# Optimization experiments

Hardware: AMD Instinct MI355X
Metric: run time of the kernel (lower is better)

Reference implementation:

```python
import jax, jax.numpy as jnp
import numpy as np
import math

N_HEAD = 16
EPS = 1e-5
GELU_C = math.sqrt(2.0 / math.pi)

def _layernorm(v, w):
    # LN with weight only (bias=None), matching the module's quirky constructor
    mu = jnp.mean(v, axis=-1, keepdims=True)
    var = jnp.mean(jnp.square(v - mu), axis=-1, keepdims=True)
    return (v - mu) * jax.lax.rsqrt(var + EPS) * w

def _new_gelu(x):
    return 0.5 * x * (1.0 + jnp.tanh(GELU_C * (x + 0.044715 * x ** 3)))

def setup_inputs() -> dict:
    key = jax.random.key(0)
    k1, k2, k3, k4 = jax.random.split(key, 4)
    B, T, C = 2, 2048, 2048
    x = jax.random.normal(k1, (B, T, C), dtype=jnp.float32)
    w_qkv = jax.random.normal(k2, (C, 3 * C), dtype=jnp.float32) * 0.02
    w1 = jax.random.normal(k3, (C, 4 * C), dtype=jnp.float32) * 0.02
    w2 = jax.random.normal(k4, (4 * C, C), dtype=jnp.float32) * 0.02
    ln_w = jnp.ones((C,), dtype=jnp.float32)
    return {"x": x, "w_qkv": w_qkv, "w1": w1, "w2": w2, "ln_w": ln_w}

def reference(x, w_qkv, w1, w2, ln_w):
    B, T, C = x.shape
    H = N_HEAD
    D = C // H
    # --- attention branch (pre-LN, shared ln weight) ---
    h = _layernorm(x, ln_w)
    qkv = h @ w_qkv  # [B,T,3C]
    q, k, v = jnp.split(qkv, 3, axis=-1)
    q = q.reshape(B, T, H, D)
    k = k.reshape(B, T, H, D)
    v = v.reshape(B, T, H, D)
    scale = 1.0 / math.sqrt(D)
    att = jnp.einsum('bthd,bshd->bhts', q, k) * scale  # [B,H,T,T]
    causal = jnp.tril(jnp.ones((T, T), dtype=bool))
    att = jnp.where(causal, att, -jnp.inf)
    att = jax.nn.softmax(att, axis=-1)
    attn_out = jnp.einsum('bhts,bshd->bthd', att, v).reshape(B, T, C)
    x = x + attn_out  # note: no output projection in this module
    # --- MLP branch (same ln weight reused) ---
    h2 = _layernorm(x, ln_w)
    mlp = _new_gelu(h2 @ w1) @ w2
    return x + mlp
```

## Files before the change

### kernel.cpp

```cpp
#include <hip/hip_runtime.h>
#include <hip/hip_bf16.h>
#include <math.h>

typedef __bf16 BF16;
typedef __attribute__((ext_vector_type(8))) __bf16 bf16x8;
typedef __attribute__((ext_vector_type(4))) float f32x4;

__device__ __forceinline__ void gld_lds16(const void* g, void* l) {
    __builtin_amdgcn_global_load_lds(
        (__attribute__((address_space(1))) void*)(const void*)g,
        (__attribute__((address_space(3))) void*)l, 16, 0, 0);
}

template <int N> __device__ __forceinline__ void vmwait() {
    asm volatile("s_waitcnt vmcnt(%0)" :: "i"(N));
}

__device__ __forceinline__ void SBAR() {
    __builtin_amdgcn_sched_barrier(0);
    __builtin_amdgcn_s_barrier();
    __builtin_amdgcn_sched_barrier(0);
}

__global__ __launch_bounds__(256) void lnorm(const float* __restrict__ x,
                                             const float* __restrict__ w,
                                             BF16* __restrict__ out) {
    const int row = blockIdx.x, tid = threadIdx.x;
    const float* xr = x + (size_t)row * 2048;
    float4 a = *(const float4*)(xr + tid * 8);
    float4 b = *(const float4*)(xr + tid * 8 + 4);
    float s1 = a.x + a.y + a.z + a.w + b.x + b.y + b.z + b.w;
    float s2 = a.x*a.x + a.y*a.y + a.z*a.z + a.w*a.w +
               b.x*b.x + b.y*b.y + b.z*b.z + b.w*b.w;
    #pragma unroll
    for (int off = 32; off; off >>= 1) {
        s1 += __shfl_xor(s1, off);
        s2 += __shfl_xor(s2, off);
    }
    __shared__ float red[8];
    const int l = tid & 63, wv = tid >> 6;
    if (l == 0) { red[wv] = s1; red[4 + wv] = s2; }
    __syncthreads();
    s1 = red[0] + red[1] + red[2] + red[3];
    s2 = red[4] + red[5] + red[6] + red[7];
    const float mean = s1 * (1.0f / 2048.0f);
    const float var  = s2 * (1.0f / 2048.0f) - mean * mean;
    const float rstd = rsqrtf(var + 1e-5f);
    float4 wa = *(const float4*)(w + tid * 8);
    float4 wb = *(const float4*)(w + tid * 8 + 4);
    bf16x8 o;
    o[0] = (BF16)((a.x - mean) * rstd * wa.x);
    o[1] = (BF16)((a.y - mean) * rstd * wa.y);
    o[2] = (BF16)((a.z - mean) * rstd * wa.z);
    o[3] = (BF16)((a.w - mean) * rstd * wa.w);
    o[4] = (BF16)((b.x - mean) * rstd * wb.x);
    o[5] = (BF16)((b.y - mean) * rstd * wb.y);
    o[6] = (BF16)((b.z - mean) * rstd * wb.z);
    o[7] = (BF16)((b.w - mean) * rstd * wb.w);
    *(bf16x8*)(out + (size_t)row * 2048 + tid * 8) = o;
}

__global__ __launch_bounds__(256) void wtrans(const float* __restrict__ W,
                                              BF16* __restrict__ Wt,
                                              int K, int N) {
    __shared__ BF16 tile[32][33];
    const int n0 = blockIdx.x * 32, k0 = blockIdx.y * 32;
    const int tx = threadIdx.x, ty = threadIdx.y;
    #pragma unroll
    for (int i = 0; i < 4; i++)
        tile[ty + 8 * i][tx] = (BF16)W[(size_t)(k0 + ty + 8 * i) * N + n0 + tx];
    __syncthreads();
    #pragma unroll
    for (int i = 0; i < 4; i++)
        Wt[(size_t)(n0 + ty + 8 * i) * K + k0 + tx] = tile[tx][ty + 8 * i];
}

__global__ __launch_bounds__(256) void vtrans(const BF16* __restrict__ qkv,
                                              BF16* __restrict__ vT) {
    __shared__ BF16 tile[32][33];
    const int t0 = blockIdx.x * 32, d0 = blockIdx.y * 32, bh = blockIdx.z;
    const int b = bh >> 4, h = bh & 15;
    const int tx = threadIdx.x, ty = threadIdx.y;
    const BF16* src = qkv + (size_t)b * 2048 * 6144 + 4096 + h * 128;
    #pragma unroll
    for (int i = 0; i < 4; i++)
        tile[ty + 8 * i][tx] = src[(size_t)(t0 + ty + 8 * i) * 6144 + d0 + tx];
    __syncthreads();
    BF16* dst = vT + (size_t)bh * 128 * 2048;
    #pragma unroll
    for (int i = 0; i < 4; i++)
        dst[(size_t)(d0 + ty + 8 * i) * 2048 + t0 + tx] = tile[tx][ty + 8 * i];
}


#define STA(SI, KK, TS) do { \
    _Pragma("unroll") \
    for (int j_ = 0; j_ < 2; ++j_) { \
        const int r_ = j_ * 128 + (tid >> 2); \
        const int sl_ = (tid & 3) ^ ((r_ >> 1) & 3); \
        gld_lds16(A + (size_t)(m0 + r_) * K + (TS) * 64 + (KK) * 32 + sl_ * 8, \
                  Ab + (SI) * 32768 + (KK) * 16384 + j_ * 8192 + w * 1024); \
    } \
} while (0)

#define STB(SI, KK, TS) do { \
    _Pragma("unroll") \
    for (int j_ = 0; j_ < LBU; ++j_) { \
        const int r_ = j_ * 128 + (tid >> 2); \
        const int sl_ = (tid & 3) ^ ((r_ >> 1) & 3); \
        gld_lds16(Bt + (size_t)(n0 + r_) * K + (TS) * 64 + (KK) * 32 + sl_ * 8, \
                  Bb + (SI) * BBUF + (KK) * (BN * 64) + j_ * 8192 + w * 1024); \
    } \
} while (0)

#define LDA(BI, MH, M_, KK) \
    (*(const bf16x8*)(Ab + (BI) * 32768 + (KK) * 16384 + \
        ((MH) * 128 + wm * 64 + (M_) * 16 + c) * 64 + ((g ^ fa) << 4)))

#define LDB(BI, N_, KK) \
    (*(const bf16x8*)(Bb + (BI) * BBUF + (KK) * (BN * 64) + \
        (wn * (BN / 4) + (N_) * 16 + c) * 64 + ((g ^ fa) << 4)))

#define MFMA_CL(MH) do { \
    __builtin_amdgcn_s_setprio(1); \
    _Pragma("unroll") \
    for (int m_ = 0; m_ < 4; ++m_) \
      _Pragma("unroll") \
      for (int n_ = 0; n_ < NR; ++n_) \
        acc[(MH) * 4 + m_][n_] = __builtin_amdgcn_mfma_f32_16x16x32_bf16( \
            af[m_], bfr[n_], acc[(MH) * 4 + m_][n_], 0, 0, 0); \
    __builtin_amdgcn_s_setprio(0); \
} while (0)

#define GBODY(BI, T, ST) do { \
    bf16x8 af[4], bfr[NR]; \
    _Pragma("unroll") for (int n_ = 0; n_ < NR; ++n_) bfr[n_] = LDB(BI, n_, 0); \
    _Pragma("unroll") for (int m_ = 0; m_ < 4; ++m_) af[m_] = LDA(BI, 0, m_, 0); \
    if (ST) STB((BI) ^ 1, 0, (T) + 1); \
    SBAR(); \
    MFMA_CL(0); \
    SBAR(); \
    _Pragma("unroll") for (int m_ = 0; m_ < 4; ++m_) af[m_] = LDA(BI, 1, m_, 0); \
    if (ST) STA((BI) ^ 1, 0, (T) + 1); \
    SBAR(); \
    MFMA_CL(1); \
    if (ST) vmwait<LBU + 2>(); else vmwait<0>(); \
    SBAR(); \
    _Pragma("unroll") for (int n_ = 0; n_ < NR; ++n_) bfr[n_] = LDB(BI, n_, 1); \
    _Pragma("unroll") for (int m_ = 0; m_ < 4; ++m_) af[m_] = LDA(BI, 0, m_, 1); \
    if (ST) STB((BI) ^ 1, 1, (T) + 1); \
    SBAR(); \
    MFMA_CL(0); \
    SBAR(); \
    _Pragma("unroll") for (int m_ = 0; m_ < 4; ++m_) af[m_] = LDA(BI, 1, m_, 1); \
    if (ST) STA((BI) ^ 1, 1, (T) + 1); \
    SBAR(); \
    MFMA_CL(1); \
    if (ST) vmwait<LBU + 2>(); \
    SBAR(); \
} while (0)

template <int MODE, int BN>
__global__ __launch_bounds__(512) void gemmT(const BF16* __restrict__ A,
                                             const BF16* __restrict__ Bt,
                                             void* __restrict__ out,
                                             const float* __restrict__ resid,
                                             int M, int N, int K) {
    constexpr int NR   = BN / 64;
    constexpr int LBU  = BN / 128;
    constexpr int BBUF = BN * 128;
    (void)M;

    extern __shared__ char smem[];
    char* const Ab = smem;
    char* const Bb = smem + 65536;

    const int tid = threadIdx.x, l = tid & 63, w = tid >> 6;
    const int wm = w >> 2, wn = w & 3;
    const int g = l >> 4, c = l & 15;
    const int fa = (c >> 1) & 3;

    const int NBX = N / BN;
    const int cpx = (int)gridDim.x >> 3;
    const int bid = (int)blockIdx.x;
    const int wg  = (bid & 7) * cpx + (bid >> 3);
    const int m0 = (wg / NBX) * 256, n0 = (wg % NBX) * BN;

    f32x4 acc[8][NR] = {};

    STB(0, 0, 0); STA(0, 0, 0); STB(0, 1, 0); STA(0, 1, 0);
    vmwait<LBU + 2>();
    SBAR();

    const int NT = K >> 6;
    for (int t = 0; t < NT - 2; t += 2) {
        GBODY(0, t, true);
        GBODY(1, t + 1, true);
    }
    GBODY(0, NT - 2, true);
    GBODY(1, NT - 1, false);

    #pragma unroll
    for (int mi = 0; mi < 8; mi++)
      #pragma unroll
      for (int ni = 0; ni < NR; ni++)
        #pragma unroll
        for (int j = 0; j < 4; j++) {
            const int row = m0 + (mi >> 2) * 128 + wm * 64 + (mi & 3) * 16 + g * 4 + j;
            const int col = n0 + wn * (BN / 4) + ni * 16 + c;
            const float v = acc[mi][ni][j];
            const size_t idx = (size_t)row * N + col;
            if (MODE == 0) {
                ((BF16*)out)[idx] = (BF16)v;
            } else if (MODE == 1) {
                const float t2 = v + 0.044715f * v * v * v;
                const float s = 1.0f / (1.0f + __expf(-1.5957691216057308f * t2));
                ((BF16*)out)[idx] = (BF16)(v * s);
            } else {
                ((float*)out)[idx] = resid[idx] + v;
            }
        }
}

__global__ __launch_bounds__(256) void attn(const BF16* __restrict__ qkv,
                                            const BF16* __restrict__ vT,
                                            const float* __restrict__ x,
                                            float* __restrict__ x2) {
    __shared__ BF16 Ks[2][64 * 128];
    __shared__ BF16 Vs[2][128 * 64];
    __shared__ BF16 Ps[4][16 * 72];
    const int tid = threadIdx.x, l = tid & 63, w = tid >> 6;
    const int g = l >> 4, c = l & 15;
    const int bid = (int)blockIdx.x;
    const int wg = (bid & 7) * 64 + (bid >> 3);
    const int pair = wg & 15, bh = wg >> 4;
    const int b = bh >> 4, h = bh & 15;
    const int xr = (c & 7) << 4;

    const BF16* qbase = qkv + (size_t)b * 2048 * 6144 + h * 128;
    const char* kbase = (const char*)(qbase + 2048);
    const char* vbase = (const char*)(vT + (size_t)bh * 128 * 2048);

    auto STAGE = [&](int bb, int k0) {
        #pragma unroll
        for (int s = 0; s < 4; ++s) {
            const int rK = (w * 4 + s) * 4 + (l >> 4);
            const int cK = ((l & 15) * 16) ^ ((rK & 7) << 4);
            gld_lds16(kbase + (size_t)(k0 + rK) * 12288 + cK,
                      &Ks[bb][(w * 4 + s) * 512]);
            const int rV = (w * 4 + s) * 8 + (l >> 3);
            const int cV = ((l & 7) * 16) ^ ((rV & 7) << 4);
            gld_lds16(vbase + (size_t)rV * 4096 + (size_t)k0 * 2 + cV,
                      &Vs[bb][(w * 4 + s) * 512]);
        }
    };

    const float scale = 0.08838834764831845f;

    #pragma unroll 1
    for (int seg = 0; seg < 2; ++seg) {
        const int qb = seg ? 31 - pair : pair;
        const int q0 = qb * 64;

        bf16x8 qf[4];
        {
            const BF16* qrow = qbase + (size_t)(q0 + w * 16 + c) * 6144 + g * 8;
            #pragma unroll
            for (int kc = 0; kc < 4; kc++)
                qf[kc] = *(const bf16x8*)(qrow + kc * 32);
        }
        float m[4]    = {-1e30f, -1e30f, -1e30f, -1e30f};
        float lsum[4] = {0.f, 0.f, 0.f, 0.f};
        f32x4 O[8] = {};

        STAGE(0, 0);
        #pragma unroll 1
        for (int kt = 0; kt <= qb; ++kt) {
            if (kt < qb) { STAGE((kt + 1) & 1, (kt + 1) * 64); vmwait<8>(); }
            else vmwait<0>();
            SBAR();
            const char* KsB = (const char*)Ks[kt & 1];
            const char* VsB = (const char*)Vs[kt & 1];

            f32x4 s4[4] = {};
            #pragma unroll
            for (int ni = 0; ni < 4; ni++)
                #pragma unroll
                for (int kc = 0; kc < 4; kc++) {
                    const bf16x8 kf = *(const bf16x8*)(KsB +
                        (ni * 16 + c) * 256 + ((kc * 64 + g * 16) ^ xr));
                    s4[ni] = __builtin_amdgcn_mfma_f32_16x16x32_bf16(
                        qf[kc], kf, s4[ni], 0, 0, 0);
                }

            const bool maskt = (kt == qb);
            float sv[4][4];
            #pragma unroll
            for (int ni = 0; ni < 4; ni++)
                #pragma unroll
                for (int j = 0; j < 4; j++) {
                    const float v = s4[ni][j] * scale;
                    sv[ni][j] = (!maskt || (ni * 16 + c <= w * 16 + g * 4 + j))
                              ? v : -1e30f;
                }

            float sf[4];
            #pragma unroll
            for (int j = 0; j < 4; j++) {
                float tm = fmaxf(fmaxf(sv[0][j], sv[1][j]),
                                 fmaxf(sv[2][j], sv[3][j]));
                tm = fmaxf(tm, __shfl_xor(tm, 1));
                tm = fmaxf(tm, __shfl_xor(tm, 2));
                tm = fmaxf(tm, __shfl_xor(tm, 4));
                tm = fmaxf(tm, __shfl_xor(tm, 8));
                const float mn = fmaxf(m[j], tm);
                sf[j] = __expf(m[j] - mn);
                m[j] = mn;
            }

            float rs[4] = {0.f, 0.f, 0.f, 0.f};
            #pragma unroll
            for (int ni = 0; ni < 4; ni++)
                #pragma unroll
                for (int j = 0; j < 4; j++) {
                    const float p = __expf(sv[ni][j] - m[j]);
                    rs[j] += p;
                    Ps[w][(g * 4 + j) * 72 + ni * 16 + c] = (BF16)p;
                }
            #pragma unroll
            for (int j = 0; j < 4; j++) {
                float t = rs[j];
                t += __shfl_xor(t, 1);
                t += __shfl_xor(t, 2);
                t += __shfl_xor(t, 4);
                t += __shfl_xor(t, 8);
                lsum[j] = lsum[j] * sf[j] + t;
            }
            #pragma unroll
            for (int dn = 0; dn < 8; dn++)
                #pragma unroll
                for (int j = 0; j < 4; j++) O[dn][j] *= sf[j];

            bf16x8 pa[2];
            #pragma unroll
            for (int ks = 0; ks < 2; ks++)
                pa[ks] = *(const bf16x8*)((const char*)Ps[w] +
                             c * 144 + ks * 64 + g * 16);
            #pragma unroll
            for (int dn = 0; dn < 8; dn++)
                #pragma unroll
                for (int ks = 0; ks < 2; ks++) {
                    const bf16x8 vf = *(const bf16x8*)(VsB +
                        (dn * 16 + c) * 128 + ((ks * 64 + g * 16) ^ xr));
                    O[dn] = __builtin_amdgcn_mfma_f32_16x16x32_bf16(
                        pa[ks], vf, O[dn], 0, 0, 0);
                }
            SBAR();
        }

        float inv[4];
        #pragma unroll
        for (int j = 0; j < 4; j++) inv[j] = 1.0f / lsum[j];
        #pragma unroll
        for (int dn = 0; dn < 8; dn++)
            #pragma unroll
            for (int j = 0; j < 4; j++) {
                const int t   = q0 + w * 16 + g * 4 + j;
                const int col = h * 128 + dn * 16 + c;
                const size_t idx = ((size_t)b * 2048 + t) * 2048 + col;
                x2[idx] = x[idx] + O[dn][j] * inv[j];
            }
    }
}

extern "C" void kernel_launch(void* const* d_in, const int* in_sizes, int n_in,
                              void* d_out, int out_size, void* d_ws, size_t ws_size,
                              hipStream_t stream) {
    const float* x     = (const float*)d_in[0];
    const float* w_qkv = (const float*)d_in[1];
    const float* w1    = (const float*)d_in[2];
    const float* w2    = (const float*)d_in[3];
    const float* ln_w  = (const float*)d_in[4];
    float* out = (float*)d_out;

    char* ws = (char*)d_ws;
    BF16* h_buf = (BF16*)ws;  ws += (size_t)4096 * 2048 * 2;
    BF16* qkvb  = (BF16*)ws;  ws += (size_t)4096 * 6144 * 2;
    BF16* vTb   = (BF16*)ws;  ws += (size_t)32 * 128 * 2048 * 2;
    BF16* wqkvT = (BF16*)ws;  ws += (size_t)6144 * 2048 * 2;
    BF16* w1T   = (BF16*)ws;  ws += (size_t)8192 * 2048 * 2;
    BF16* w2T   = (BF16*)ws;  ws += (size_t)2048 * 8192 * 2;
    BF16* mlp1  = (BF16*)ws;  ws += (size_t)4096 * 8192 * 2;

    hipFuncSetAttribute((const void*)&gemmT<0, 256>,
                        hipFuncAttributeMaxDynamicSharedMemorySize, 131072);
    hipFuncSetAttribute((const void*)&gemmT<1, 256>,
                        hipFuncAttributeMaxDynamicSharedMemorySize, 131072);
    hipFuncSetAttribute((const void*)&gemmT<2, 128>,
                        hipFuncAttributeMaxDynamicSharedMemorySize, 98304);

    lnorm<<<4096, 256, 0, stream>>>(x, ln_w, h_buf);
    wtrans<<<dim3(192, 64), dim3(32, 8), 0, stream>>>(w_qkv, wqkvT, 2048, 6144);
    gemmT<0, 256><<<384, 512, 131072, stream>>>(
        h_buf, wqkvT, qkvb, nullptr, 4096, 6144, 2048);
    vtrans<<<dim3(64, 4, 32), dim3(32, 8), 0, stream>>>(qkvb, vTb);
    attn<<<512, 256, 0, stream>>>(qkvb, vTb, x, out);

    lnorm<<<4096, 256, 0, stream>>>(out, ln_w, h_buf);
    wtrans<<<dim3(256, 64), dim3(32, 8), 0, stream>>>(w1, w1T, 2048, 8192);
    gemmT<1, 256><<<512, 512, 131072, stream>>>(
        h_buf, w1T, mlp1, nullptr, 4096, 8192, 2048);
    wtrans<<<dim3(64, 256), dim3(32, 8), 0, stream>>>(w2, w2T, 8192, 2048);
    gemmT<2, 128><<<256, 512, 98304, stream>>>(
        mlp1, w2T, out, out, 4096, 2048, 8192);
}
```

Baseline: 560.2 us.

## Restructure GEMM into four-stage LDS pipeline with single barrier per k-step

Replaces the double-buffered GEMM (64-wide k-steps split into M-half MFMA clusters with many barriers and priority hints) with a 4-deep ring of 32-wide k-slices, issuing loads three stages ahead and synchronizing once per stage. The tile is parameterized by BM with a fixed 256-wide N, changing the down-projection's tile shape to 128x256. The aim is deeper memory latency hiding and less barrier overhead. In exchange it drops setprio scheduling and uses smaller per-stage MFMA batches.

Measured after the change: 550.9 us, median of 2. About the same (-1.6%).

```diff
diff --git a/kernel.cpp b/kernel.cpp
--- a/kernel.cpp
+++ b/kernel.cpp
@@ -14,12 +14,6 @@
 
 template <int N> __device__ __forceinline__ void vmwait() {
     asm volatile("s_waitcnt vmcnt(%0)" :: "i"(N));
-}
-
-__device__ __forceinline__ void SBAR() {
-    __builtin_amdgcn_sched_barrier(0);
-    __builtin_amdgcn_s_barrier();
-    __builtin_amdgcn_sched_barrier(0);
 }
 
 __global__ __launch_bounds__(256) void lnorm(const float* __restrict__ x,
@@ -93,121 +87,106 @@
 }
 
 
-#define STA(SI, KK, TS) do { \
+#define STA(SI, TS) do { \
+    _Pragma("unroll") \
+    for (int j_ = 0; j_ < LA; ++j_) { \
+        const int r_ = j_ * 128 + (tid >> 2); \
+        const int sl_ = (tid & 3) ^ ((r_ >> 1) & 3); \
+        gld_lds16(A + (size_t)(m0 + r_) * K + (TS) * 32 + sl_ * 8, \
+                  Ab + (SI) * ABUF + j_ * 8192 + w * 1024); \
+    } \
+} while (0)
+
+#define STB(SI, TS) do { \
     _Pragma("unroll") \
     for (int j_ = 0; j_ < 2; ++j_) { \
         const int r_ = j_ * 128 + (tid >> 2); \
         const int sl_ = (tid & 3) ^ ((r_ >> 1) & 3); \
-        gld_lds16(A + (size_t)(m0 + r_) * K + (TS) * 64 + (KK) * 32 + sl_ * 8, \
-                  Ab + (SI) * 32768 + (KK) * 16384 + j_ * 8192 + w * 1024); \
+        gld_lds16(Bt + (size_t)(n0 + r_) * K + (TS) * 32 + sl_ * 8, \
+                  Bb + (SI) * 16384 + j_ * 8192 + w * 1024); \
     } \
 } while (0)
 
-#define STB(SI, KK, TS) do { \
+#define LDA(BI, M_) \
+    (*(const bf16x8*)(Ab + (BI) * ABUF + \
+        (wm * (BM / 2) + (M_) * 16 + c) * 64 + ((g ^ fa) << 4)))
+
+#define LDB(BI, N_) \
+    (*(const bf16x8*)(Bb + (BI) * 16384 + \
+        (wn * 64 + (N_) * 16 + c) * 64 + ((g ^ fa) << 4)))
+
+#define GB(BI, T, DS, VW) do { \
+    bf16x8 af[MR], bfr[4]; \
+    _Pragma("unroll") for (int n_ = 0; n_ < 4; ++n_) bfr[n_] = LDB(BI, n_); \
+    _Pragma("unroll") for (int m_ = 0; m_ < MR; ++m_) af[m_] = LDA(BI, m_); \
+    if (DS) { STB(((BI) + 3) & 3, (T) + 3); STA(((BI) + 3) & 3, (T) + 3); } \
     _Pragma("unroll") \
-    for (int j_ = 0; j_ < LBU; ++j_) { \
-        const int r_ = j_ * 128 + (tid >> 2); \
-        const int sl_ = (tid & 3) ^ ((r_ >> 1) & 3); \
-        gld_lds16(Bt + (size_t)(n0 + r_) * K + (TS) * 64 + (KK) * 32 + sl_ * 8, \
-                  Bb + (SI) * BBUF + (KK) * (BN * 64) + j_ * 8192 + w * 1024); \
-    } \
+    for (int m_ = 0; m_ < MR; ++m_) \
+      _Pragma("unroll") \
+      for (int n_ = 0; n_ < 4; ++n_) \
+        acc[m_][n_] = __builtin_amdgcn_mfma_f32_16x16x32_bf16( \
+            af[m_], bfr[n_], acc[m_][n_], 0, 0, 0); \
+    vmwait<(VW)>(); \
+    __builtin_amdgcn_s_barrier(); \
+    __builtin_amdgcn_sched_barrier(0); \
 } while (0)
 
-#define LDA(BI, MH, M_, KK) \
-    (*(const bf16x8*)(Ab + (BI) * 32768 + (KK) * 16384 + \
-        ((MH) * 128 + wm * 64 + (M_) * 16 + c) * 64 + ((g ^ fa) << 4)))
-
-#define LDB(BI, N_, KK) \
-    (*(const bf16x8*)(Bb + (BI) * BBUF + (KK) * (BN * 64) + \
-        (wn * (BN / 4) + (N_) * 16 + c) * 64 + ((g ^ fa) << 4)))
-
-#define MFMA_CL(MH) do { \
-    __builtin_amdgcn_s_setprio(1); \
-    _Pragma("unroll") \
-    for (int m_ = 0; m_ < 4; ++m_) \
-      _Pragma("unroll") \
-      for (int n_ = 0; n_ < NR; ++n_) \
-        acc[(MH) * 4 + m_][n_] = __builtin_amdgcn_mfma_f32_16x16x32_bf16( \
-            af[m_], bfr[n_], acc[(MH) * 4 + m_][n_], 0, 0, 0); \
-    __builtin_amdgcn_s_setprio(0); \
-} while (0)
-
-#define GBODY(BI, T, ST) do { \
-    bf16x8 af[4], bfr[NR]; \
-    _Pragma("unroll") for (int n_ = 0; n_ < NR; ++n_) bfr[n_] = LDB(BI, n_, 0); \
-    _Pragma("unroll") for (int m_ = 0; m_ < 4; ++m_) af[m_] = LDA(BI, 0, m_, 0); \
-    if (ST) STB((BI) ^ 1, 0, (T) + 1); \
-    SBAR(); \
-    MFMA_CL(0); \
-    SBAR(); \
-    _Pragma("unroll") for (int m_ = 0; m_ < 4; ++m_) af[m_] = LDA(BI, 1, m_, 0); \
-    if (ST) STA((BI) ^ 1, 0, (T) + 1); \
-    SBAR(); \
-    MFMA_CL(1); \
-    if (ST) vmwait<LBU + 2>(); else vmwait<0>(); \
-    SBAR(); \
-    _Pragma("unroll") for (int n_ = 0; n_ < NR; ++n_) bfr[n_] = LDB(BI, n_, 1); \
-    _Pragma("unroll") for (int m_ = 0; m_ < 4; ++m_) af[m_] = LDA(BI, 0, m_, 1); \
-    if (ST) STB((BI) ^ 1, 1, (T) + 1); \
-    SBAR(); \
-    MFMA_CL(0); \
-    SBAR(); \
-    _Pragma("unroll") for (int m_ = 0; m_ < 4; ++m_) af[m_] = LDA(BI, 1, m_, 1); \
-    if (ST) STA((BI) ^ 1, 1, (T) + 1); \
-    SBAR(); \
-    MFMA_CL(1); \
-    if (ST) vmwait<LBU + 2>(); \
-    SBAR(); \
-} while (0)
-
-template <int MODE, int BN>
-__global__ __launch_bounds__(512) void gemmT(const BF16* __restrict__ A,
+template <int MODE, int BM>
+__global__ __launch_bounds__(512) void gemmN(const BF16* __restrict__ A,
                                              const BF16* __restrict__ Bt,
                                              void* __restrict__ out,
                                              const float* __restrict__ resid,
                                              int M, int N, int K) {
-    constexpr int NR   = BN / 64;
-    constexpr int LBU  = BN / 128;
-    constexpr int BBUF = BN * 128;
+    constexpr int MR   = BM / 32;
+    constexpr int LA   = BM / 128;
+    constexpr int LPT  = LA + 2;
+    constexpr int ABUF = BM * 64;
     (void)M;
 
     extern __shared__ char smem[];
     char* const Ab = smem;
-    char* const Bb = smem + 65536;
+    char* const Bb = smem + 4 * ABUF;
 
     const int tid = threadIdx.x, l = tid & 63, w = tid >> 6;
     const int wm = w >> 2, wn = w & 3;
     const int g = l >> 4, c = l & 15;
     const int fa = (c >> 1) & 3;
 
-    const int NBX = N / BN;
+    const int NBX = N >> 8;
     const int cpx = (int)gridDim.x >> 3;
     const int bid = (int)blockIdx.x;
     const int wg  = (bid & 7) * cpx + (bid >> 3);
-    const int m0 = (wg / NBX) * 256, n0 = (wg % NBX) * BN;
-
-    f32x4 acc[8][NR] = {};
-
-    STB(0, 0, 0); STA(0, 0, 0); STB(0, 1, 0); STA(0, 1, 0);
-    vmwait<LBU + 2>();
-    SBAR();
-
-    const int NT = K >> 6;
-    for (int t = 0; t < NT - 2; t += 2) {
-        GBODY(0, t, true);
-        GBODY(1, t + 1, true);
+    const int m0 = (wg / NBX) * BM, n0 = (wg % NBX) * 256;
+
+    f32x4 acc[MR][4] = {};
+
+    STB(0, 0); STA(0, 0);
+    STB(1, 1); STA(1, 1);
+    STB(2, 2); STA(2, 2);
+    vmwait<2 * LPT>();
+    __builtin_amdgcn_s_barrier();
+    __builtin_amdgcn_sched_barrier(0);
+
+    const int NT = K >> 5;
+    for (int t = 0; t < NT - 4; t += 4) {
+        GB(0, t,     1, 2 * LPT);
+        GB(1, t + 1, 1, 2 * LPT);
+        GB(2, t + 2, 1, 2 * LPT);
+        GB(3, t + 3, 1, 2 * LPT);
     }
-    GBODY(0, NT - 2, true);
-    GBODY(1, NT - 1, false);
-
-    #pragma unroll
-    for (int mi = 0; mi < 8; mi++)
+    GB(0, NT - 4, 1, 2 * LPT);
+    GB(1, NT - 3, 0, LPT);
+    GB(2, NT - 2, 0, 0);
+    GB(3, NT - 1, 0, 0);
+
+    #pragma unroll
+    for (int mi = 0; mi < MR; mi++)
       #pragma unroll
-      for (int ni = 0; ni < NR; ni++)
+      for (int ni = 0; ni < 4; ni++)
         #pragma unroll
         for (int j = 0; j < 4; j++) {
-            const int row = m0 + (mi >> 2) * 128 + wm * 64 + (mi & 3) * 16 + g * 4 + j;
-            const int col = n0 + wn * (BN / 4) + ni * 16 + c;
+            const int row = m0 + wm * (BM / 2) + mi * 16 + g * 4 + j;
+            const int col = n0 + wn * 64 + ni * 16 + c;
             const float v = acc[mi][ni][j];
             const size_t idx = (size_t)row * N + col;
             if (MODE == 0) {
@@ -278,7 +257,8 @@
         for (int kt = 0; kt <= qb; ++kt) {
             if (kt < qb) { STAGE((kt + 1) & 1, (kt + 1) * 64); vmwait<8>(); }
             else vmwait<0>();
-            SBAR();
+            __builtin_amdgcn_s_barrier();
+            __builtin_amdgcn_sched_barrier(0);
             const char* KsB = (const char*)Ks[kt & 1];
             const char* VsB = (const char*)Vs[kt & 1];
 
@@ -355,7 +335,8 @@
                     O[dn] = __builtin_amdgcn_mfma_f32_16x16x32_bf16(
                         pa[ks], vf, O[dn], 0, 0, 0);
                 }
-            SBAR();
+            __builtin_amdgcn_s_barrier();
+            __builtin_amdgcn_sched_barrier(0);
         }
 
         float inv[4];
@@ -392,25 +373,25 @@
     BF16* w2T   = (BF16*)ws;  ws += (size_t)2048 * 8192 * 2;
     BF16* mlp1  = (BF16*)ws;  ws += (size_t)4096 * 8192 * 2;
 
-    hipFuncSetAttribute((const void*)&gemmT<0, 256>,
+    hipFuncSetAttribute((const void*)&gemmN<0, 256>,
                         hipFuncAttributeMaxDynamicSharedMemorySize, 131072);
-    hipFuncSetAttribute((const void*)&gemmT<1, 256>,
+    hipFuncSetAttribute((const void*)&gemmN<1, 256>,
                         hipFuncAttributeMaxDynamicSharedMemorySize, 131072);
-    hipFuncSetAttribute((const void*)&gemmT<2, 128>,
+    hipFuncSetAttribute((const void*)&gemmN<2, 128>,
                         hipFuncAttributeMaxDynamicSharedMemorySize, 98304);
 
     lnorm<<<4096, 256, 0, stream>>>(x, ln_w, h_buf);
     wtrans<<<dim3(192, 64), dim3(32, 8), 0, stream>>>(w_qkv, wqkvT, 2048, 6144);
-    gemmT<0, 256><<<384, 512, 131072, stream>>>(
+    gemmN<0, 256><<<384, 512, 131072, stream>>>(
         h_buf, wqkvT, qkvb, nullptr, 4096, 6144, 2048);
     vtrans<<<dim3(64, 4, 32), dim3(32, 8), 0, stream>>>(qkvb, vTb);
     attn<<<512, 256, 0, stream>>>(qkvb, vTb, x, out);
 
     lnorm<<<4096, 256, 0, stream>>>(out, ln_w, h_buf);
     wtrans<<<dim3(256, 64), dim3(32, 8), 0, stream>>>(w1, w1T, 2048, 8192);
-    gemmT<1, 256><<<512, 512, 131072, stream>>>(
+    gemmN<1, 256><<<512, 512, 131072, stream>>>(
         h_buf, w1T, mlp1, nullptr, 4096, 8192, 2048);
     wtrans<<<dim3(64, 256), dim3(32, 8), 0, stream>>>(w2, w2T, 8192, 2048);
-    gemmT<2, 128><<<256, 512, 98304, stream>>>(
+    gemmN<2, 128><<<256, 512, 98304, stream>>>(
         mlp1, w2T, out, out, 4096, 2048, 8192);
 }
```
